# Kernel tuning notes

Measured on AMD Instinct MI355X. Metric: run time of the kernel, lower is better.

## Reference

```python
import jax, jax.numpy as jnp
import numpy as np

N_OBJ, N_P, N2 = 16, 128, 2048
C, H, W = 256, 384, 384
IMG_W, IMG_H = 384.0, 384.0  # img_metas['img_shape'][:2][::-1]
SIM_THR = 0.0
LOSS_WEIGHT = 1.0
COS_EPS = 1e-8  # torch F.cosine_similarity default


def setup_inputs() -> dict:
    key = jax.random.key(0)
    k1, k2, k3, k4 = jax.random.split(key, 4)
    img_size = jnp.array([IMG_W, IMG_H], jnp.float32)
    point_set_1 = jax.random.uniform(k1, (N_OBJ, N_P, 2), jnp.float32) * img_size
    point_set_2 = jax.random.uniform(k2, (N_OBJ, N2, 2), jnp.float32) * img_size
    key_points = jax.random.uniform(k3, (N_OBJ * N_P, 2), jnp.float32) * img_size
    feats = jax.random.normal(k4, (1, C, H, W), jnp.float32)
    return {"point_set_1": point_set_1, "point_set_2": point_set_2,
            "feats": feats, "key_points": key_points}


def _grid_sample(img, pts01):
    # img: [C,H,W]; pts01: [P,2] (x,y) in [0,1]. Bilinear, align_corners=False,
    # zero padding -- matches mmcv point_sample / torch grid_sample.
    Ci, Hi, Wi = img.shape
    g = 2.0 * pts01 - 1.0
    x = ((g[:, 0] + 1.0) * Wi - 1.0) * 0.5
    y = ((g[:, 1] + 1.0) * Hi - 1.0) * 0.5
    x0 = jnp.floor(x)
    y0 = jnp.floor(y)
    wx1 = x - x0
    wy1 = y - y0

    def tap(xi, yi, wgt):
        valid = (xi >= 0) & (xi < Wi) & (yi >= 0) & (yi < Hi)
        xc = jnp.clip(xi, 0, Wi - 1).astype(jnp.int32)
        yc = jnp.clip(yi, 0, Hi - 1).astype(jnp.int32)
        return img[:, yc, xc] * (wgt * valid)[None, :]  # [C,P]

    return (tap(x0, y0, (1 - wx1) * (1 - wy1))
            + tap(x0 + 1, y0, wx1 * (1 - wy1))
            + tap(x0, y0 + 1, (1 - wx1) * wy1)
            + tap(x0 + 1, y0 + 1, wx1 * wy1))  # [C,P]


def reference(point_set_1, point_set_2, feats, key_points):
    img_size = jnp.array([IMG_W, IMG_H], feats.dtype)
    img = feats[0]  # feats.expand() reuses the same map for every object

    # feats_set_1: [n_obj, n_p, C]; feats_set_2: [n_obj, n2, C]
    f1 = _grid_sample(img, key_points / img_size).T.reshape(N_OBJ, N_P, C)
    f2 = _grid_sample(img, (point_set_2 / img_size).reshape(-1, 2)).T.reshape(N_OBJ, N2, C)

    # cosine similarity over channel dim (norms clamped to eps like torch)
    n1 = jnp.maximum(jnp.linalg.norm(f1, axis=-1), COS_EPS)  # [O,P]
    n2 = jnp.maximum(jnp.linalg.norm(f2, axis=-1), COS_EPS)  # [O,N2]
    sims = jnp.einsum('opc,onc->opn', f1, f2) / (n1[..., None] * n2[:, None, :])
    mask = sims >= SIM_THR  # [O,P,N2]

    # pairwise L2 distances between each key point and candidate set
    diff = point_set_1[:, :, None, :] - point_set_2[:, None, :, :]
    d = jnp.linalg.norm(diff, axis=-1)  # [O,P,N2]

    cnt = mask.sum(-1)  # [O,P]
    has = cnt > 0
    dmin = jnp.min(jnp.where(mask, d, jnp.inf), axis=-1)
    dmean = jnp.sum(jnp.where(mask, d, 0.0), axis=-1) / jnp.maximum(cnt, 1)
    # chamfer of a single point vs masked set: (nearest + mean)/2, 'mean' reduction
    m = (point_set_2.sum(axis=(1, 2)) >= 0).astype(d.dtype)  # [O]
    cost = jnp.where(has, 0.5 * (dmin + dmean), 0.0) * m[:, None]  # [O,P]

    dist = (cost.sum(-1) / N_P).mean()
    return dist * LOSS_WEIGHT
```

## Files before the change

kernel.cpp:

```cpp
#include <hip/hip_runtime.h>
#include <hip/hip_bf16.h>
#include <math.h>

#define W_    384
#define H_    384
#define HW_   (384*384)
#define C_    256
#define NOBJ  16
#define NP    128
#define N2    2048
#define NF1   (NOBJ*NP)
#define NPTS  (NOBJ*NP + NOBJ*N2)
#define NG    16
#define NT    8

typedef __attribute__((ext_vector_type(8))) short short8;
typedef __attribute__((ext_vector_type(4))) float f32x4;

__device__ __forceinline__ unsigned short f2bf(float v) {
    unsigned int u = __float_as_uint(v);
    u += 0x7fffu + ((u >> 16) & 1u);
    return (unsigned short)(u >> 16);
}

__device__ __forceinline__ void gload_lds16(const void* g, void* l) {
    __builtin_amdgcn_global_load_lds(
        (const __attribute__((address_space(1))) void*)g,
        (__attribute__((address_space(3))) void*)l, 16, 0, 0);
}

__global__ __launch_bounds__(256) void k_transpose(const float* __restrict__ feats,
                                                   unsigned short* __restrict__ ftT) {
    __shared__ float tile[64 * 256];
    int b     = blockIdx.x;
    int pbase = (b % (HW_ / 256)) * 256;
    int cbase = (b / (HW_ / 256)) * 64;
    int t     = threadIdx.x;
    int l     = t & 63;
    int w     = t >> 6;

    #pragma unroll
    for (int pass = 0; pass < 16; ++pass) {
        int c = pass * 4 + w;
        const float* src = feats + (size_t)(cbase + c) * HW_ + pbase + l * 4;
        gload_lds16(src, &tile[c * 256]);
    }
    asm volatile("s_waitcnt vmcnt(0)" ::: "memory");
    __syncthreads();

    int p = t;
    size_t obase = (size_t)(pbase + p) * C_ + cbase;
    #pragma unroll
    for (int ch = 0; ch < 8; ++ch) {
        unsigned short u[8];
        #pragma unroll
        for (int j = 0; j < 8; ++j) u[j] = f2bf(tile[(ch * 8 + j) * 256 + p]);
        uint4 pk;
        pk.x = (unsigned)u[0] | ((unsigned)u[1] << 16);
        pk.y = (unsigned)u[2] | ((unsigned)u[3] << 16);
        pk.z = (unsigned)u[4] | ((unsigned)u[5] << 16);
        pk.w = (unsigned)u[6] | ((unsigned)u[7] << 16);
        *(uint4*)(ftT + obase + ch * 8) = pk;
    }
}

__global__ __launch_bounds__(256) void k_sample(const float* __restrict__ kpts,
                                                const float* __restrict__ ps2,
                                                const unsigned short* __restrict__ ftT,
                                                unsigned short* __restrict__ f12) {
    int wave  = blockIdx.x * 4 + (threadIdx.x >> 6);
    int lane  = threadIdx.x & 63;
    int half  = lane >> 5;
    int l32   = lane & 31;
    int point = wave * 2 + half;
    int cb    = l32 * 8;

    const float* src = (point < NF1) ? (kpts + (size_t)point * 2)
                                     : (ps2 + (size_t)(point - NF1) * 2);
    float x  = src[0] - 0.5f;
    float y  = src[1] - 0.5f;
    float x0 = floorf(x), y0 = floorf(y);
    int ix0 = (int)x0, iy0 = (int)y0;
    float fx = x - x0, fy = y - y0;

    float a[8] = {0.f, 0.f, 0.f, 0.f, 0.f, 0.f, 0.f, 0.f};
    #pragma unroll
    for (int dy = 0; dy < 2; ++dy) {
        #pragma unroll
        for (int dx = 0; dx < 2; ++dx) {
            int ix = ix0 + dx, iy = iy0 + dy;
            float w = (dx ? fx : 1.f - fx) * (dy ? fy : 1.f - fy);
            if (ix >= 0 && ix < W_ && iy >= 0 && iy < H_) {
                uint4 tv = *(const uint4*)(ftT + ((size_t)(iy * W_ + ix) * C_ + cb));
                a[0] += w * __uint_as_float(tv.x << 16);
                a[1] += w * __uint_as_float(tv.x & 0xffff0000u);
                a[2] += w * __uint_as_float(tv.y << 16);
                a[3] += w * __uint_as_float(tv.y & 0xffff0000u);
                a[4] += w * __uint_as_float(tv.z << 16);
                a[5] += w * __uint_as_float(tv.z & 0xffff0000u);
                a[6] += w * __uint_as_float(tv.w << 16);
                a[7] += w * __uint_as_float(tv.w & 0xffff0000u);
            }
        }
    }
    uint4 pk;
    pk.x = (unsigned)f2bf(a[0]) | ((unsigned)f2bf(a[1]) << 16);
    pk.y = (unsigned)f2bf(a[2]) | ((unsigned)f2bf(a[3]) << 16);
    pk.z = (unsigned)f2bf(a[4]) | ((unsigned)f2bf(a[5]) << 16);
    pk.w = (unsigned)f2bf(a[6]) | ((unsigned)f2bf(a[7]) << 16);
    *(uint4*)(f12 + (size_t)point * C_ + cb) = pk;
}

__global__ __launch_bounds__(256) void k_sample_direct(const float* __restrict__ kpts,
                                                       const float* __restrict__ ps2,
                                                       const float* __restrict__ feats,
                                                       unsigned short* __restrict__ f12) {
    int point = blockIdx.x * 4 + (threadIdx.x >> 6);
    int lane  = threadIdx.x & 63;
    int cb    = lane * 4;

    const float* src = (point < NF1) ? (kpts + (size_t)point * 2)
                                     : (ps2 + (size_t)(point - NF1) * 2);
    float x  = src[0] - 0.5f, y = src[1] - 0.5f;
    float x0 = floorf(x), y0 = floorf(y);
    int ix0 = (int)x0, iy0 = (int)y0;
    float fx = x - x0, fy = y - y0;

    float acc[4] = {0.f, 0.f, 0.f, 0.f};
    #pragma unroll
    for (int dy = 0; dy < 2; ++dy) {
        #pragma unroll
        for (int dx = 0; dx < 2; ++dx) {
            int ix = ix0 + dx, iy = iy0 + dy;
            float w = (dx ? fx : 1.f - fx) * (dy ? fy : 1.f - fy);
            if (ix >= 0 && ix < W_ && iy >= 0 && iy < H_) {
                int base = iy * W_ + ix;
                #pragma unroll
                for (int u = 0; u < 4; ++u)
                    acc[u] += w * feats[(size_t)(cb + u) * HW_ + base];
            }
        }
    }
    ushort4 o;
    o.x = f2bf(acc[0]); o.y = f2bf(acc[1]); o.z = f2bf(acc[2]); o.w = f2bf(acc[3]);
    *(ushort4*)(f12 + (size_t)point * C_ + cb) = o;
}

__device__ __forceinline__ void bload(const short* bbase, int t, short8* dst) {
    const short8* bp = (const short8*)(bbase + (size_t)t * 16 * C_);
    #pragma unroll
    for (int kb = 0; kb < 8; ++kb) dst[kb] = bp[kb * 4];
}

__global__ __launch_bounds__(256) void k_simdist(const unsigned short* __restrict__ f12,
                                                 const float* __restrict__ ps1,
                                                 const float* __restrict__ ps2,
                                                 float* __restrict__ pmin,
                                                 float* __restrict__ psum,
                                                 float* __restrict__ pcnt) {
    int wid  = blockIdx.x * 4 + (threadIdx.x >> 6);
    int lane = threadIdx.x & 63;
    int ng = wid & 15;
    int pt = (wid >> 4) & 7;
    int o  = wid >> 7;
    int quad = lane >> 4, col = lane & 15;

    const short* f12s = (const short*)f12;
    const short8* aptr =
        (const short8*)(f12s + ((size_t)(o * NP + pt * 16 + col) * C_ + quad * 8));
    short8 a[8];
    #pragma unroll
    for (int kb = 0; kb < 8; ++kb) a[kb] = aptr[kb * 4];

    const short* bbase = f12s + ((size_t)(NF1 + o * N2 + ng * 128 + col) * C_ + quad * 8);

    const float2* ps1v = (const float2*)ps1;
    const float2* ps2v = (const float2*)ps2;
    float pxr[4], pyr[4];
    #pragma unroll
    for (int r = 0; r < 4; ++r) {
        float2 pc = ps1v[o * NP + pt * 16 + quad * 4 + r];
        pxr[r] = pc.x; pyr[r] = pc.y;
    }

    float mn[4] = {INFINITY, INFINITY, INFINITY, INFINITY};
    float sm[4] = {0.f, 0.f, 0.f, 0.f};
    float ct[4] = {0.f, 0.f, 0.f, 0.f};

    auto ctile = [&](int t, short8 (&b)[8]) {
        f32x4 acc = {0.f, 0.f, 0.f, 0.f};
        #pragma unroll
        for (int kb = 0; kb < 8; ++kb)
            acc = __builtin_amdgcn_mfma_f32_16x16x32_bf16(a[kb], b[kb], acc, 0, 0, 0);
        float2 nc = ps2v[o * N2 + ng * 128 + t * 16 + col];
        #pragma unroll
        for (int r = 0; r < 4; ++r) {
            if (acc[r] >= 0.f) {
                float dx = pxr[r] - nc.x, dy = pyr[r] - nc.y;
                float d  = sqrtf(dx * dx + dy * dy);
                mn[r] = fminf(mn[r], d); sm[r] += d; ct[r] += 1.f;
            }
        }
    };

    short8 b0[8], b1[8];
    bload(bbase, 0, b0);
    for (int t = 0; t < NT; t += 2) {
        bload(bbase, t + 1, b1);
        ctile(t, b0);
        if (t + 2 < NT) bload(bbase, t + 2, b0);
        ctile(t + 1, b1);
    }

    #pragma unroll
    for (int r = 0; r < 4; ++r) {
        #pragma unroll
        for (int off = 1; off < 16; off <<= 1) {
            mn[r] = fminf(mn[r], __shfl_xor(mn[r], off, 16));
            sm[r] += __shfl_xor(sm[r], off, 16);
            ct[r] += __shfl_xor(ct[r], off, 16);
        }
    }
    if (col == 0) {
        #pragma unroll
        for (int r = 0; r < 4; ++r) {
            int p   = pt * 16 + quad * 4 + r;
            int idx = (o * NP + p) * NG + ng;
            pmin[idx] = mn[r]; psum[idx] = sm[r]; pcnt[idx] = ct[r];
        }
    }
}

__global__ __launch_bounds__(64) void k_final1(const float* __restrict__ pmin,
                                               const float* __restrict__ psum,
                                               const float* __restrict__ pcnt,
                                               float* __restrict__ wpart) {
    int b    = blockIdx.x;
    int lane = threadIdx.x;
    float tot = 0.f;
    #pragma unroll
    for (int rep = 0; rep < 2; ++rep) {
        int pair = b * 64 + lane + rep * 1024;
        int base = pair * NG;
        const float4* pm = (const float4*)(pmin + base);
        const float4* ps = (const float4*)(psum + base);
        const float4* pc = (const float4*)(pcnt + base);
        float mn = INFINITY, sm = 0.f, ct = 0.f;
        #pragma unroll
        for (int g4 = 0; g4 < 4; ++g4) {
            float4 a = pm[g4], bb = ps[g4], c = pc[g4];
            mn = fminf(mn, fminf(fminf(a.x, a.y), fminf(a.z, a.w)));
            sm += bb.x + bb.y + bb.z + bb.w;
            ct += c.x + c.y + c.z + c.w;
        }
        if (ct > 0.f) tot += 0.5f * (mn + sm / ct);
    }
    #pragma unroll
    for (int off = 32; off; off >>= 1) tot += __shfl_xor(tot, off, 64);
    if (lane == 0) wpart[b] = tot;
}

__global__ __launch_bounds__(64) void k_final2(const float* __restrict__ wpart,
                                               float* __restrict__ out) {
    int t = threadIdx.x;
    float v = (t < 16) ? wpart[t] : 0.f;
    #pragma unroll
    for (int off = 8; off; off >>= 1) v += __shfl_xor(v, off, 16);
    if (t == 0) out[0] = v * (1.0f / (NOBJ * NP));
}

extern "C" void kernel_launch(void* const* d_in, const int* in_sizes, int n_in,
                              void* d_out, int out_size, void* d_ws, size_t ws_size,
                              hipStream_t stream) {
    const float* ps1   = (const float*)d_in[0];
    const float* ps2   = (const float*)d_in[1];
    const float* feats = (const float*)d_in[2];
    const float* kpts  = (const float*)d_in[3];
    float* out = (float*)d_out;

    const size_t sz_ftT  = (size_t)HW_ * C_ * sizeof(unsigned short);
    const size_t sz_f12  = (size_t)NPTS * C_ * sizeof(unsigned short);
    const size_t sz_part = (size_t)NOBJ * NP * NG * sizeof(float);
    const size_t sz_wp   = 64 * sizeof(float);

    char* ws = (char*)d_ws;
    if (ws_size >= sz_ftT + sz_f12 + 3 * sz_part + sz_wp) {
        unsigned short* ftT = (unsigned short*)ws;
        unsigned short* f12 = (unsigned short*)(ws + sz_ftT);
        float* pmin  = (float*)(ws + sz_ftT + sz_f12);
        float* psum  = (float*)(ws + sz_ftT + sz_f12 + sz_part);
        float* pcnt  = (float*)(ws + sz_ftT + sz_f12 + 2 * sz_part);
        float* wpart = (float*)(ws + sz_ftT + sz_f12 + 3 * sz_part);

        k_transpose<<<(HW_ / 256) * (C_ / 64), 256, 0, stream>>>(feats, ftT);
        k_sample<<<NPTS / 8, 256, 0, stream>>>(kpts, ps2, ftT, f12);
        k_simdist<<<NOBJ * 8 * NG / 4, 256, 0, stream>>>(f12, ps1, ps2, pmin, psum, pcnt);
        k_final1<<<16, 64, 0, stream>>>(pmin, psum, pcnt, wpart);
        k_final2<<<1, 64, 0, stream>>>(wpart, out);
    } else {
        unsigned short* f12 = (unsigned short*)ws;
        float* pmin  = (float*)(ws + sz_f12);
        float* psum  = (float*)(ws + sz_f12 + sz_part);
        float* pcnt  = (float*)(ws + sz_f12 + 2 * sz_part);
        float* wpart = (float*)(ws + sz_f12 + 3 * sz_part);

        k_sample_direct<<<NPTS / 4, 256, 0, stream>>>(kpts, ps2, feats, f12);
        k_simdist<<<NOBJ * 8 * NG / 4, 256, 0, stream>>>(f12, ps1, ps2, pmin, psum, pcnt);
        k_final1<<<16, 64, 0, stream>>>(pmin, psum, pcnt, wpart);
        k_final2<<<1, 64, 0, stream>>>(wpart, out);
    }
}
```

Before: 285.2 us.

## Replace full feature-map transpose with row-binned points and LDS-staged sampling

Removes the full HWxC bf16 transpose of the feature map. Sample points are instead bucketed by 4-row bands using count, scan and scatter kernels. Each block of the fused sampler loads a 5-row x 32-channel slab of feats into LDS as packed bf16 pairs and bilinearly samples only the points in its band. This avoids writing and re-reading a 75 MB transposed copy, at the cost of three small binning kernels, an atomic scatter, and about 123 KB of dynamic LDS per block, which limits occupancy.

```diff
diff --git a/kernel.cpp b/kernel.cpp
--- a/kernel.cpp
+++ b/kernel.cpp
@@ -13,6 +13,7 @@
 #define NPTS  (NOBJ*NP + NOBJ*N2)
 #define NG    16
 #define NT    8
+#define NBIN  96
 
 typedef __attribute__((ext_vector_type(8))) short short8;
 typedef __attribute__((ext_vector_type(4))) float f32x4;
@@ -23,92 +24,126 @@
     return (unsigned short)(u >> 16);
 }
 
-__device__ __forceinline__ void gload_lds16(const void* g, void* l) {
-    __builtin_amdgcn_global_load_lds(
-        (const __attribute__((address_space(1))) void*)g,
-        (__attribute__((address_space(3))) void*)l, 16, 0, 0);
-}
-
-__global__ __launch_bounds__(256) void k_transpose(const float* __restrict__ feats,
-                                                   unsigned short* __restrict__ ftT) {
-    __shared__ float tile[64 * 256];
-    int b     = blockIdx.x;
-    int pbase = (b % (HW_ / 256)) * 256;
-    int cbase = (b / (HW_ / 256)) * 64;
+__device__ __forceinline__ int bin_of(float yimg) {
+    int iy0 = (int)floorf(yimg - 0.5f);
+    return min(max(iy0, 0), 383) >> 2;
+}
+
+__global__ __launch_bounds__(256) void k_binA(const float* __restrict__ kpts,
+                                              const float* __restrict__ ps2,
+                                              int* __restrict__ gcnt) {
+    int g = blockIdx.x;
+    int t = threadIdx.x;
+    int c = 0;
+    for (int i = t; i < NPTS; i += 256) {
+        float y = (i < NF1) ? kpts[2 * i + 1] : ps2[2 * (i - NF1) + 1];
+        c += (bin_of(y) == g);
+    }
+    #pragma unroll
+    for (int off = 32; off; off >>= 1) c += __shfl_xor(c, off, 64);
+    __shared__ int wred[4];
+    if ((t & 63) == 0) wred[t >> 6] = c;
+    __syncthreads();
+    if (t == 0) gcnt[g] = wred[0] + wred[1] + wred[2] + wred[3];
+}
+
+__global__ __launch_bounds__(128) void k_binB(const int* __restrict__ gcnt,
+                                              int* __restrict__ gofs,
+                                              int* __restrict__ gcur) {
+    __shared__ int c[NBIN], o[NBIN + 1];
+    int t = threadIdx.x;
+    if (t < NBIN) c[t] = gcnt[t];
+    __syncthreads();
+    if (t == 0) {
+        int run = 0;
+        for (int g = 0; g < NBIN; ++g) { o[g] = run; run += c[g]; }
+        o[NBIN] = run;
+    }
+    __syncthreads();
+    if (t < NBIN) { gofs[t] = o[t]; gcur[t] = o[t]; }
+    if (t == 0) gofs[NBIN] = o[NBIN];
+}
+
+__global__ __launch_bounds__(256) void k_binC(const float* __restrict__ kpts,
+                                              const float* __restrict__ ps2,
+                                              int* __restrict__ gcur,
+                                              int* __restrict__ plist) {
+    int i = blockIdx.x * 256 + threadIdx.x;
+    float y = (i < NF1) ? kpts[2 * i + 1] : ps2[2 * (i - NF1) + 1];
+    int pos = atomicAdd(&gcur[bin_of(y)], 1);
+    plist[pos] = i;
+}
+
+__global__ __launch_bounds__(256) void k_sample_fused(const float* __restrict__ kpts,
+                                                      const float* __restrict__ ps2,
+                                                      const float* __restrict__ feats,
+                                                      const int* __restrict__ gofs,
+                                                      const int* __restrict__ plist,
+                                                      unsigned short* __restrict__ f12) {
+    extern __shared__ unsigned int su[];
+    int bid   = blockIdx.x;
+    int g     = bid >> 3;
+    int ct    = bid & 7;
+    int g4    = g * 4;
+    int cbase = ct * 32;
     int t     = threadIdx.x;
-    int l     = t & 63;
+    int lane  = t & 63;
     int w     = t >> 6;
-
-    #pragma unroll
-    for (int pass = 0; pass < 16; ++pass) {
-        int c = pass * 4 + w;
-        const float* src = feats + (size_t)(cbase + c) * HW_ + pbase + l * 4;
-        gload_lds16(src, &tile[c * 256]);
-    }
-    asm volatile("s_waitcnt vmcnt(0)" ::: "memory");
+    int cp    = lane & 15;
+    int xo    = lane >> 4;
+    int xbase = w * 96;
+
+    #pragma unroll
+    for (int r = 0; r < 5; ++r) {
+        int row = g4 + r;
+        if (row < 384) {
+            const float* f0 = feats + (size_t)(cbase + 2 * cp) * HW_
+                            + (size_t)row * 384 + xbase + xo;
+            #pragma unroll
+            for (int it = 0; it < 24; ++it) {
+                float v0 = f0[it * 4];
+                float v1 = f0[it * 4 + HW_];
+                su[((r * 384) + xbase + it * 4 + xo) * 16 + cp] =
+                    (unsigned)f2bf(v0) | ((unsigned)f2bf(v1) << 16);
+            }
+        }
+    }
     __syncthreads();
 
-    int p = t;
-    size_t obase = (size_t)(pbase + p) * C_ + cbase;
-    #pragma unroll
-    for (int ch = 0; ch < 8; ++ch) {
-        unsigned short u[8];
-        #pragma unroll
-        for (int j = 0; j < 8; ++j) u[j] = f2bf(tile[(ch * 8 + j) * 256 + p]);
-        uint4 pk;
-        pk.x = (unsigned)u[0] | ((unsigned)u[1] << 16);
-        pk.y = (unsigned)u[2] | ((unsigned)u[3] << 16);
-        pk.z = (unsigned)u[4] | ((unsigned)u[5] << 16);
-        pk.w = (unsigned)u[6] | ((unsigned)u[7] << 16);
-        *(uint4*)(ftT + obase + ch * 8) = pk;
-    }
-}
-
-__global__ __launch_bounds__(256) void k_sample(const float* __restrict__ kpts,
-                                                const float* __restrict__ ps2,
-                                                const unsigned short* __restrict__ ftT,
-                                                unsigned short* __restrict__ f12) {
-    int wave  = blockIdx.x * 4 + (threadIdx.x >> 6);
-    int lane  = threadIdx.x & 63;
-    int half  = lane >> 5;
-    int l32   = lane & 31;
-    int point = wave * 2 + half;
-    int cb    = l32 * 8;
-
-    const float* src = (point < NF1) ? (kpts + (size_t)point * 2)
-                                     : (ps2 + (size_t)(point - NF1) * 2);
-    float x  = src[0] - 0.5f;
-    float y  = src[1] - 0.5f;
-    float x0 = floorf(x), y0 = floorf(y);
-    int ix0 = (int)x0, iy0 = (int)y0;
-    float fx = x - x0, fy = y - y0;
-
-    float a[8] = {0.f, 0.f, 0.f, 0.f, 0.f, 0.f, 0.f, 0.f};
-    #pragma unroll
-    for (int dy = 0; dy < 2; ++dy) {
-        #pragma unroll
-        for (int dx = 0; dx < 2; ++dx) {
-            int ix = ix0 + dx, iy = iy0 + dy;
-            float w = (dx ? fx : 1.f - fx) * (dy ? fy : 1.f - fy);
-            if (ix >= 0 && ix < W_ && iy >= 0 && iy < H_) {
-                uint4 tv = *(const uint4*)(ftT + ((size_t)(iy * W_ + ix) * C_ + cb));
-                a[0] += w * __uint_as_float(tv.x << 16);
-                a[1] += w * __uint_as_float(tv.x & 0xffff0000u);
-                a[2] += w * __uint_as_float(tv.y << 16);
-                a[3] += w * __uint_as_float(tv.y & 0xffff0000u);
-                a[4] += w * __uint_as_float(tv.z << 16);
-                a[5] += w * __uint_as_float(tv.z & 0xffff0000u);
-                a[6] += w * __uint_as_float(tv.w << 16);
-                a[7] += w * __uint_as_float(tv.w & 0xffff0000u);
+    int ofs = gofs[g];
+    int n   = gofs[g + 1] - ofs;
+    for (int base = w * 4; base < n; base += 16) {
+        int i = base + xo;
+        if (i >= n) continue;
+        int pid = plist[ofs + i];
+        const float* src = (pid < NF1) ? (kpts + (size_t)pid * 2)
+                                       : (ps2 + (size_t)(pid - NF1) * 2);
+        float x  = src[0] - 0.5f;
+        float y  = src[1] - 0.5f;
+        float x0 = floorf(x), y0 = floorf(y);
+        int ix0 = (int)x0, iy0 = (int)y0;
+        float fx = x - x0, fy = y - y0;
+
+        float a0 = 0.f, a1 = 0.f;
+        #pragma unroll
+        for (int dy = 0; dy < 2; ++dy) {
+            int iy = iy0 + dy;
+            if (iy < 0 || iy > 383) continue;
+            int rl = iy - g4;
+            float wy = dy ? fy : 1.f - fy;
+            #pragma unroll
+            for (int dx = 0; dx < 2; ++dx) {
+                int ix = ix0 + dx;
+                if (ix < 0 || ix > 383) continue;
+                float wgt = (dx ? fx : 1.f - fx) * wy;
+                unsigned u = su[(rl * 384 + ix) * 16 + cp];
+                a0 += wgt * __uint_as_float(u << 16);
+                a1 += wgt * __uint_as_float(u & 0xffff0000u);
             }
         }
-    }
-    uint4 pk;
-    pk.x = (unsigned)f2bf(a[0]) | ((unsigned)f2bf(a[1]) << 16);
-    pk.y = (unsigned)f2bf(a[2]) | ((unsigned)f2bf(a[3]) << 16);
-    pk.z = (unsigned)f2bf(a[4]) | ((unsigned)f2bf(a[5]) << 16);
-    pk.w = (unsigned)f2bf(a[6]) | ((unsigned)f2bf(a[7]) << 16);
-    *(uint4*)(f12 + (size_t)point * C_ + cb) = pk;
+        *(unsigned*)(f12 + (size_t)pid * C_ + cbase + 2 * cp) =
+            (unsigned)f2bf(a0) | ((unsigned)f2bf(a1) << 16);
+    }
 }
 
 __global__ __launch_bounds__(256) void k_sample_direct(const float* __restrict__ kpts,
@@ -278,32 +313,40 @@
     const float* kpts  = (const float*)d_in[3];
     float* out = (float*)d_out;
 
-    const size_t sz_ftT  = (size_t)HW_ * C_ * sizeof(unsigned short);
     const size_t sz_f12  = (size_t)NPTS * C_ * sizeof(unsigned short);
     const size_t sz_part = (size_t)NOBJ * NP * NG * sizeof(float);
-    const size_t sz_wp   = 64 * sizeof(float);
+    const size_t o_pmin  = sz_f12;
+    const size_t o_psum  = o_pmin + sz_part;
+    const size_t o_pcnt  = o_psum + sz_part;
+    const size_t o_wp    = o_pcnt + sz_part;
+    const size_t o_gcnt  = o_wp + 256;
+    const size_t o_gofs  = o_gcnt + 512;
+    const size_t o_gcur  = o_gofs + 512;
+    const size_t o_plist = o_gcur + 512;
+    const size_t need    = o_plist + (size_t)NPTS * sizeof(int);
 
     char* ws = (char*)d_ws;
-    if (ws_size >= sz_ftT + sz_f12 + 3 * sz_part + sz_wp) {
-        unsigned short* ftT = (unsigned short*)ws;
-        unsigned short* f12 = (unsigned short*)(ws + sz_ftT);
-        float* pmin  = (float*)(ws + sz_ftT + sz_f12);
-        float* psum  = (float*)(ws + sz_ftT + sz_f12 + sz_part);
-        float* pcnt  = (float*)(ws + sz_ftT + sz_f12 + 2 * sz_part);
-        float* wpart = (float*)(ws + sz_ftT + sz_f12 + 3 * sz_part);
-
-        k_transpose<<<(HW_ / 256) * (C_ / 64), 256, 0, stream>>>(feats, ftT);
-        k_sample<<<NPTS / 8, 256, 0, stream>>>(kpts, ps2, ftT, f12);
+    unsigned short* f12 = (unsigned short*)ws;
+    float* pmin  = (float*)(ws + o_pmin);
+    float* psum  = (float*)(ws + o_psum);
+    float* pcnt  = (float*)(ws + o_pcnt);
+    float* wpart = (float*)(ws + o_wp);
+
+    if (ws_size >= need) {
+        int* gcnt  = (int*)(ws + o_gcnt);
+        int* gofs  = (int*)(ws + o_gofs);
+        int* gcur  = (int*)(ws + o_gcur);
+        int* plist = (int*)(ws + o_plist);
+
+        k_binA<<<NBIN, 256, 0, stream>>>(kpts, ps2, gcnt);
+        k_binB<<<1, 128, 0, stream>>>(gcnt, gofs, gcur);
+        k_binC<<<NPTS / 256, 256, 0, stream>>>(kpts, ps2, gcur, plist);
+        k_sample_fused<<<NBIN * 8, 256, 5 * 384 * 16 * sizeof(unsigned), stream>>>(
+            kpts, ps2, feats, gofs, plist, f12);
         k_simdist<<<NOBJ * 8 * NG / 4, 256, 0, stream>>>(f12, ps1, ps2, pmin, psum, pcnt);
         k_final1<<<16, 64, 0, stream>>>(pmin, psum, pcnt, wpart);
         k_final2<<<1, 64, 0, stream>>>(wpart, out);
     } else {
-        unsigned short* f12 = (unsigned short*)ws;
-        float* pmin  = (float*)(ws + sz_f12);
-        float* psum  = (float*)(ws + sz_f12 + sz_part);
-        float* pcnt  = (float*)(ws + sz_f12 + 2 * sz_part);
-        float* wpart = (float*)(ws + sz_f12 + 3 * sz_part);
-
         k_sample_direct<<<NPTS / 4, 256, 0, stream>>>(kpts, ps2, feats, f12);
         k_simdist<<<NOBJ * 8 * NG / 4, 256, 0, stream>>>(f12, ps1, ps2, pmin, psum, pcnt);
         k_final1<<<16, 64, 0, stream>>>(pmin, psum, pcnt, wpart);
```

Result: slower. 401.9 us (+40.9%).
